# Kernel optimization log

Measured on AMD Instinct MI355X. Metric: run time of the kernel, lower is better.

The kernel has to match this reference:

```python
import jax, jax.numpy as jnp
import numpy as np

N_LAYERS = 3
B = 524288
PI = np.float32(np.pi)
INV_SQRT2 = np.float32(1.0 / np.sqrt(2.0))
H_GATE = (INV_SQRT2 * np.array([[1, 1], [1, -1]])).astype(np.complex64)
H_GATE = jnp.asarray(H_GATE)

# wire 0 = most significant bit (PennyLane convention)
_IDX = np.arange(16)
BITS = [(( _IDX >> (3 - w)) & 1).astype(np.float32) for w in range(4)]  # [16] each

def _cnot_perm(c, t):
    ctrl = (_IDX >> (3 - c)) & 1
    return _IDX ^ (ctrl << (3 - t))
CNOT_PERMS = {(c, t): jnp.asarray(_cnot_perm(c, t)) for c in range(4) for t in range(4) if c != t}

def apply_h(state, w):
    # state: [B,16] complex64
    s = state.reshape(-1, 2, 2, 2, 2)
    s = jnp.moveaxis(jnp.moveaxis(s, 1 + w, 4) @ H_GATE, 4, 1 + w)
    return s.reshape(-1, 16)

def apply_rz(state, w, theta):
    # RZ(theta) = diag(exp(-i theta/2), exp(+i theta/2)); theta: [B]
    sign = jnp.asarray(2.0 * BITS[w] - 1.0)  # [16] in {-1,+1}
    phase = jnp.exp(0.5j * theta[:, None] * sign[None, :])
    return state * phase

def apply_cnot(state, c, t):
    return state[:, CNOT_PERMS[(c, t)]]

ZZ_PAIRS = [(0, 1), (1, 2), (2, 3), (3, 0)]

def embed(state, x):
    # QuantumEmbedding(x), x: [B,4]
    for _ in range(N_LAYERS):
        for j in range(4):
            state = apply_h(state, j)
            state = apply_rz(state, j, -2.0 * x[:, j])
        for a, b in ZZ_PAIRS:
            state = apply_cnot(state, a, b)
            state = apply_rz(state, b, -2.0 * (PI - x[:, a]) * (PI - x[:, b]))
            state = apply_cnot(state, a, b)
    return state

def embed_adjoint(state, x):
    # adjoint(QuantumEmbedding)(x): reverse gate order, negate RZ angles
    for _ in range(N_LAYERS):
        for a, b in reversed(ZZ_PAIRS):
            state = apply_cnot(state, a, b)
            state = apply_rz(state, b, 2.0 * (PI - x[:, a]) * (PI - x[:, b]))
            state = apply_cnot(state, a, b)
        for j in reversed(range(4)):
            state = apply_rz(state, j, 2.0 * x[:, j])
            state = apply_h(state, j)
    return state

def mlp(x, W1, b1, W2, b2, W3, b3):
    h1 = jax.nn.relu(x @ W1 + b1)
    h2 = jax.nn.relu(h1 @ W2 + b2)
    return h2 @ W3 + b3

def setup_inputs() -> dict:
    key = jax.random.key(0)
    ks = jax.random.split(key, 8)
    return {
        'x1': jax.random.normal(ks[0], (B, 4), jnp.float32),
        'x2': jax.random.normal(ks[1], (B, 4), jnp.float32),
        'W1': jax.random.normal(ks[2], (4, 8), jnp.float32) * 0.5,
        'b1': jax.random.normal(ks[3], (8,), jnp.float32) * 0.1,
        'W2': jax.random.normal(ks[4], (8, 8), jnp.float32) * 0.35,
        'b2': jax.random.normal(ks[5], (8,), jnp.float32) * 0.1,
        'W3': jax.random.normal(ks[6], (8, 4), jnp.float32) * 0.35,
        'b3': jax.random.normal(ks[7], (4,), jnp.float32) * 0.1,
    }

def reference(x1, x2, W1, b1, W2, b2, W3, b3):
    f1 = mlp(x1, W1, b1, W2, b2, W3, b3)  # [B,4]
    f2 = mlp(x2, W1, b1, W2, b2, W3, b3)  # [B,4]
    state = jnp.zeros((f1.shape[0], 16), jnp.complex64).at[:, 0].set(1.0)
    state = embed(state, f1)
    state = embed_adjoint(state, f2)
    amp0 = state[:, 0]
    return amp0.real ** 2 + amp0.imag ** 2  # probs(|0000>) == fidelity, [B]
```

## Files before the change

### kernel.cpp

```cpp
#include <hip/hip_runtime.h>
#include <math.h>


#define PI_F 3.14159265358979323846f

__device__ __forceinline__ void fast_sincos(float x, float& s, float& c) {
    const float INV2PI = 0.15915494309189535f;
    const float TWOPI  = 6.283185307179586f;
    float k = rintf(x * INV2PI);
    float r = fmaf(-k, TWOPI, x);
    s = __sinf(r);
    c = __cosf(r);
}

__device__ __forceinline__ void phase_table(const float f[4], float cs[16], float sn[16]) {
    float g0 = PI_F - f[0], g1 = PI_F - f[1], g2 = PI_F - f[2], g3 = PI_F - f[3];
    float p01 = g0 * g1, p12 = g1 * g2, p23 = g2 * g3, p30 = g3 * g0;
#pragma unroll
    for (int s = 0; s < 16; ++s) {
        const float s0 = (s & 8) ? 1.f : -1.f;
        const float s1 = (s & 4) ? 1.f : -1.f;
        const float s2 = (s & 2) ? 1.f : -1.f;
        const float s3 = (s & 1) ? 1.f : -1.f;
        float phi = -(f[0] * s0 + f[1] * s1 + f[2] * s2 + f[3] * s3)
                  + p01 * (s0 * s1) + p12 * (s1 * s2)
                  + p23 * (s2 * s3) + p30 * (s3 * s0);
        float sv, cv;
        fast_sincos(phi, sv, cv);
        sn[s] = 0.25f * sv;
        cs[s] = 0.25f * cv;
    }
}

__device__ __forceinline__ void run_circuit(const float cs[16], const float sn[16],
                                            float re[16], float im[16]) {
#pragma unroll
    for (int s = 0; s < 16; ++s) { re[s] = cs[s]; im[s] = sn[s]; }
#pragma unroll
    for (int layer = 1; layer < 3; ++layer) {
#pragma unroll
        for (int m = 1; m < 16; m <<= 1) {
#pragma unroll
            for (int s = 0; s < 16; ++s) {
                if (!(s & m)) {
                    float ar = re[s], br = re[s | m];
                    re[s] = ar + br; re[s | m] = ar - br;
                    float ai = im[s], bi = im[s | m];
                    im[s] = ai + bi; im[s | m] = ai - bi;
                }
            }
        }
#pragma unroll
        for (int s = 0; s < 16; ++s) {
            float r = re[s] * cs[s] - im[s] * sn[s];
            float i = re[s] * sn[s] + im[s] * cs[s];
            re[s] = r; im[s] = i;
        }
    }
}

__device__ __forceinline__ void mlp_dual(
    const float xa[4], const float xb[4],
    const float* __restrict__ W1, const float* __restrict__ b1,
    const float* __restrict__ W2, const float* __restrict__ b2,
    const float* __restrict__ W3, const float* __restrict__ b3,
    float fa[4], float fb[4]) {
    float h1a[8], h1b[8];
#pragma unroll
    for (int k = 0; k < 8; ++k) {
        float aa = b1[k], ab = aa;
#pragma unroll
        for (int j = 0; j < 4; ++j) {
            float w = W1[j * 8 + k];
            aa = fmaf(xa[j], w, aa);
            ab = fmaf(xb[j], w, ab);
        }
        h1a[k] = fmaxf(aa, 0.f);
        h1b[k] = fmaxf(ab, 0.f);
    }
    float h2a[8], h2b[8];
#pragma unroll
    for (int k = 0; k < 8; ++k) {
        float aa = b2[k], ab = aa;
#pragma unroll
        for (int j = 0; j < 8; ++j) {
            float w = W2[j * 8 + k];
            aa = fmaf(h1a[j], w, aa);
            ab = fmaf(h1b[j], w, ab);
        }
        h2a[k] = fmaxf(aa, 0.f);
        h2b[k] = fmaxf(ab, 0.f);
    }
#pragma unroll
    for (int k = 0; k < 4; ++k) {
        float aa = b3[k], ab = aa;
#pragma unroll
        for (int j = 0; j < 8; ++j) {
            float w = W3[j * 4 + k];
            aa = fmaf(h2a[j], w, aa);
            ab = fmaf(h2b[j], w, ab);
        }
        fa[k] = aa;
        fb[k] = ab;
    }
}

__global__ __launch_bounds__(256) void fidelity_kernel(
    const float* __restrict__ x1, const float* __restrict__ x2,
    const float* __restrict__ W1, const float* __restrict__ b1,
    const float* __restrict__ W2, const float* __restrict__ b2,
    const float* __restrict__ W3, const float* __restrict__ b3,
    float* __restrict__ out, int n) {
    int tid = blockIdx.x * 256 + threadIdx.x;
    if (tid >= n) return;

    float4 a4 = ((const float4*)x1)[tid];
    float4 b4 = ((const float4*)x2)[tid];
    float xa[4] = {a4.x, a4.y, a4.z, a4.w};
    float xb[4] = {b4.x, b4.y, b4.z, b4.w};

    float fa[4], fb[4];
    mlp_dual(xa, xb, W1, b1, W2, b2, W3, b3, fa, fb);

    float cs[16], sn[16];
    float re1[16], im1[16];
    phase_table(fa, cs, sn);
    run_circuit(cs, sn, re1, im1);

    float re2[16], im2[16];
    phase_table(fb, cs, sn);
    run_circuit(cs, sn, re2, im2);

    float dr = 0.f, di = 0.f;
#pragma unroll
    for (int s = 0; s < 16; ++s) {
        dr = fmaf(re2[s], re1[s], dr);
        dr = fmaf(im2[s], im1[s], dr);
        di = fmaf(re2[s], im1[s], di);
        di = fmaf(-im2[s], re1[s], di);
    }
    out[tid] = dr * dr + di * di;
}

extern "C" void kernel_launch(void* const* d_in, const int* in_sizes, int n_in,
                              void* d_out, int out_size, void* d_ws, size_t ws_size,
                              hipStream_t stream) {
    const float* x1 = (const float*)d_in[0];
    const float* x2 = (const float*)d_in[1];
    const float* W1 = (const float*)d_in[2];
    const float* b1 = (const float*)d_in[3];
    const float* W2 = (const float*)d_in[4];
    const float* b2 = (const float*)d_in[5];
    const float* W3 = (const float*)d_in[6];
    const float* b3 = (const float*)d_in[7];
    float* out = (float*)d_out;

    int n = out_size;
    int block = 256;
    int grid = (n + block - 1) / block;
    fidelity_kernel<<<grid, block, 0, stream>>>(x1, x2, W1, b1, W2, b2, W3, b3, out, n);
}
```

Measured before the change: 94.20 us.

## Apply adjoint circuit directly to state instead of computing two states and inner product

Instead of simulating both embedded states separately and taking their inner product, the kernel now runs the forward circuit and then applies the adjoint circuit (conjugate phase multiplies plus Walsh-Hadamard transforms) to the same state. The final amplitude of |0000> is the sum of the amplitudes, scaled once at the end instead of with a 0.25 factor per phase. This keeps a single 32-register state live instead of two, which may lower register pressure and raise occupancy. The trade is two extra WHT passes plus one extra diagonal multiply. The linear phase terms are also precomputed in pairs to save a few operations per entry.

```diff
diff --git a/kernel.cpp b/kernel.cpp
--- a/kernel.cpp
+++ b/kernel.cpp
@@ -16,46 +16,50 @@
 __device__ __forceinline__ void phase_table(const float f[4], float cs[16], float sn[16]) {
     float g0 = PI_F - f[0], g1 = PI_F - f[1], g2 = PI_F - f[2], g3 = PI_F - f[3];
     float p01 = g0 * g1, p12 = g1 * g2, p23 = g2 * g3, p30 = g3 * g0;
+    float u = f[0] + f[1], v = f[0] - f[1];
+    float lin01[4] = {u, v, -v, -u};
+    float w = f[2] + f[3], z = f[2] - f[3];
+    float lin23[4] = {w, z, -z, -w};
 #pragma unroll
     for (int s = 0; s < 16; ++s) {
         const float s0 = (s & 8) ? 1.f : -1.f;
         const float s1 = (s & 4) ? 1.f : -1.f;
         const float s2 = (s & 2) ? 1.f : -1.f;
         const float s3 = (s & 1) ? 1.f : -1.f;
-        float phi = -(f[0] * s0 + f[1] * s1 + f[2] * s2 + f[3] * s3)
+        float phi = lin01[(s >> 2) & 3] + lin23[s & 3]
                   + p01 * (s0 * s1) + p12 * (s1 * s2)
                   + p23 * (s2 * s3) + p30 * (s3 * s0);
-        float sv, cv;
-        fast_sincos(phi, sv, cv);
-        sn[s] = 0.25f * sv;
-        cs[s] = 0.25f * cv;
+        fast_sincos(phi, sn[s], cs[s]);
     }
 }
 
-__device__ __forceinline__ void run_circuit(const float cs[16], const float sn[16],
-                                            float re[16], float im[16]) {
+__device__ __forceinline__ void wht16(float a[16]) {
 #pragma unroll
-    for (int s = 0; s < 16; ++s) { re[s] = cs[s]; im[s] = sn[s]; }
+    for (int m = 1; m < 16; m <<= 1) {
 #pragma unroll
-    for (int layer = 1; layer < 3; ++layer) {
-#pragma unroll
-        for (int m = 1; m < 16; m <<= 1) {
-#pragma unroll
-            for (int s = 0; s < 16; ++s) {
-                if (!(s & m)) {
-                    float ar = re[s], br = re[s | m];
-                    re[s] = ar + br; re[s | m] = ar - br;
-                    float ai = im[s], bi = im[s | m];
-                    im[s] = ai + bi; im[s | m] = ai - bi;
-                }
+        for (int s = 0; s < 16; ++s) {
+            if (!(s & m)) {
+                float x = a[s], y = a[s | m];
+                a[s] = x + y; a[s | m] = x - y;
             }
         }
+    }
+}
+
+template <bool CONJ>
+__device__ __forceinline__ void diag_mul(float re[16], float im[16],
+                                         const float cs[16], const float sn[16]) {
 #pragma unroll
-        for (int s = 0; s < 16; ++s) {
-            float r = re[s] * cs[s] - im[s] * sn[s];
-            float i = re[s] * sn[s] + im[s] * cs[s];
-            re[s] = r; im[s] = i;
+    for (int s = 0; s < 16; ++s) {
+        float r, i;
+        if (CONJ) {
+            r = fmaf(re[s], cs[s],  im[s] * sn[s]);
+            i = fmaf(im[s], cs[s], -re[s] * sn[s]);
+        } else {
+            r = fmaf(re[s], cs[s], -im[s] * sn[s]);
+            i = fmaf(im[s], cs[s],  re[s] * sn[s]);
         }
+        re[s] = r; im[s] = i;
     }
 }
 
@@ -71,9 +75,9 @@
         float aa = b1[k], ab = aa;
 #pragma unroll
         for (int j = 0; j < 4; ++j) {
-            float w = W1[j * 8 + k];
-            aa = fmaf(xa[j], w, aa);
-            ab = fmaf(xb[j], w, ab);
+            float wv = W1[j * 8 + k];
+            aa = fmaf(xa[j], wv, aa);
+            ab = fmaf(xb[j], wv, ab);
         }
         h1a[k] = fmaxf(aa, 0.f);
         h1b[k] = fmaxf(ab, 0.f);
@@ -84,9 +88,9 @@
         float aa = b2[k], ab = aa;
 #pragma unroll
         for (int j = 0; j < 8; ++j) {
-            float w = W2[j * 8 + k];
-            aa = fmaf(h1a[j], w, aa);
-            ab = fmaf(h1b[j], w, ab);
+            float wv = W2[j * 8 + k];
+            aa = fmaf(h1a[j], wv, aa);
+            ab = fmaf(h1b[j], wv, ab);
         }
         h2a[k] = fmaxf(aa, 0.f);
         h2b[k] = fmaxf(ab, 0.f);
@@ -96,9 +100,9 @@
         float aa = b3[k], ab = aa;
 #pragma unroll
         for (int j = 0; j < 8; ++j) {
-            float w = W3[j * 4 + k];
-            aa = fmaf(h2a[j], w, aa);
-            ab = fmaf(h2b[j], w, ab);
+            float wv = W3[j * 4 + k];
+            aa = fmaf(h2a[j], wv, aa);
+            ab = fmaf(h2b[j], wv, ab);
         }
         fa[k] = aa;
         fb[k] = ab;
@@ -123,23 +127,31 @@
     mlp_dual(xa, xb, W1, b1, W2, b2, W3, b3, fa, fb);
 
     float cs[16], sn[16];
-    float re1[16], im1[16];
+    float re[16], im[16];
+
     phase_table(fa, cs, sn);
-    run_circuit(cs, sn, re1, im1);
+#pragma unroll
+    for (int s = 0; s < 16; ++s) { re[s] = cs[s]; im[s] = sn[s]; }
+#pragma unroll
+    for (int l = 0; l < 2; ++l) {
+        wht16(re); wht16(im);
+        diag_mul<false>(re, im, cs, sn);
+    }
 
-    float re2[16], im2[16];
     phase_table(fb, cs, sn);
-    run_circuit(cs, sn, re2, im2);
+    diag_mul<true>(re, im, cs, sn);
+#pragma unroll
+    for (int l = 0; l < 2; ++l) {
+        wht16(re); wht16(im);
+        diag_mul<true>(re, im, cs, sn);
+    }
 
     float dr = 0.f, di = 0.f;
 #pragma unroll
-    for (int s = 0; s < 16; ++s) {
-        dr = fmaf(re2[s], re1[s], dr);
-        dr = fmaf(im2[s], im1[s], dr);
-        di = fmaf(re2[s], im1[s], di);
-        di = fmaf(-im2[s], re1[s], di);
-    }
-    out[tid] = dr * dr + di * di;
+    for (int s = 0; s < 16; ++s) { dr += re[s]; di += im[s]; }
+    const float SC = 1.0f / 4096.0f;
+    dr *= SC; di *= SC;
+    out[tid] = fmaf(dr, dr, di * di);
 }
 
 extern "C" void kernel_launch(void* const* d_in, const int* in_sizes, int n_in,
```

After: 95.73 us. About the same (+1.6%).
